# Performance work log

Measured on AMD Instinct MI355X. Metric: run time of the kernel, lower is better.

## Reference

```python
import jax, jax.numpy as jnp
import numpy as np

ALPHA = 0.02
NEG = -9e15

def lrelu(x):
    return jnp.where(x >= 0, x, ALPHA * x)

def layer_norm(x, eps=1e-5):
    m = jnp.mean(x, axis=-1, keepdims=True)
    v = jnp.var(x, axis=-1, keepdims=True)
    return (x - m) * jax.lax.rsqrt(v + eps)

def setup_inputs() -> dict:
    key = jax.random.key(0)
    ks = jax.random.split(key, 10)
    B, N, F_IN, D = 8, 2048, 10, 128
    h = jax.random.normal(ks[0], (B, N, F_IN), jnp.float32)
    adj = jax.random.randint(ks[1], (B, N, N), 0, 2, jnp.int32)
    s = 0.1
    return {
        "h": h,
        "adj": adj,
        "W1": jax.random.normal(ks[2], (D, F_IN), jnp.float32) * s,
        "b1": jax.random.normal(ks[3], (D,), jnp.float32) * s,
        "Wg": jax.random.normal(ks[4], (D, D), jnp.float32) * s,
        "bg": jax.random.normal(ks[5], (D,), jnp.float32) * s,
        "a1": jax.random.normal(ks[6], (D,), jnp.float32) * s,
        "a2": jax.random.normal(ks[7], (D,), jnp.float32) * s,
        "W2": jax.random.normal(ks[8], (2, D), jnp.float32) * s,
        "b2": jax.random.normal(ks[9], (2,), jnp.float32) * s,
    }

def reference(h, adj, W1, b1, Wg, bg, a1, a2, W2, b2):
    # fc1 + layernorm + leakyrelu
    x = h @ W1.T + b1                      # [B,N,128]
    x = lrelu(layer_norm(x))
    # GAT layer
    Wh = x @ Wg.T + bg                     # [B,N,128]
    e1 = Wh @ a1                           # [B,N]
    e2 = Wh @ a2                           # [B,N]
    e = lrelu(e1[:, :, None] + e2[:, None, :])  # [B,N,N]
    e = jnp.where(adj != 0, e, NEG)
    attn = jax.nn.softmax(e, axis=2)
    hp = jnp.einsum('bij,bjd->bid', attn, Wh)    # [B,N,128]
    hp = lrelu(layer_norm(hp))
    # global max pool over nodes
    pooled = jnp.max(hp, axis=1)           # [B,128]
    out = pooled @ W2.T + b2               # [B,2]
    return jax.nn.log_softmax(out, axis=-1)
```

## Files before the change

### kernel.cpp

```cpp
#include <hip/hip_runtime.h>

#define B 8
#define N 2048
#define FIN 10
#define D 128
#define ALPHA 0.02f
#define BR 32
#define TI 32
#define JC 128
#define NBLK_ATTN ((N / TI) * B)

typedef short bf8 __attribute__((ext_vector_type(8)));
typedef short s4v __attribute__((ext_vector_type(4)));
typedef float f32x4 __attribute__((ext_vector_type(4)));

__device__ __forceinline__ float lrelu(float x) { return x >= 0.f ? x : ALPHA * x; }

__device__ __forceinline__ short f2b(float f) {
    unsigned u = __float_as_uint(f);
    return (short)((u + 0x7fffu + ((u >> 16) & 1u)) >> 16);
}

__device__ __forceinline__ float b2f(short s) {
    return __uint_as_float(((unsigned)(unsigned short)s) << 16);
}

__device__ __forceinline__ unsigned enc_key(float v) {
    unsigned b = __float_as_uint(v);
    return (b & 0x80000000u) ? ~b : (b | 0x80000000u);
}
__device__ __forceinline__ float dec_key(unsigned k) {
    unsigned b = (k & 0x80000000u) ? (k & 0x7fffffffu) : ~k;
    return __uint_as_float(b);
}

__global__ __launch_bounds__(256) void k_proj(
    const float* __restrict__ h, const float* __restrict__ W1, const float* __restrict__ b1,
    const float* __restrict__ Wg, const float* __restrict__ bg,
    const float* __restrict__ a1, const float* __restrict__ a2,
    unsigned short* __restrict__ WhT, float* __restrict__ e1g, float* __restrict__ e2g,
    unsigned* __restrict__ pooled, unsigned* __restrict__ cnt)
{
    __shared__ __align__(16) short xep_lds[32 * 136];
    __shared__ __align__(16) short wg_lds[D * 136];
    __shared__ float W1_lds[D * 11];
    __shared__ float h_lds[BR * FIN];
    __shared__ float ep1[2][BR], ep2[2][BR];

    const int t = threadIdx.x;
    const int r0 = blockIdx.x * BR;
    const int bb = r0 >> 11;
    const int jloc = r0 & (N - 1);

    if (blockIdx.x < B && t < D) pooled[blockIdx.x * D + t] = 0u;
    if (blockIdx.x == 0 && t == 128) *cnt = 0u;

    for (int idx = t; idx < D * FIN; idx += 256)
        W1_lds[(idx / FIN) * 11 + (idx % FIN)] = W1[idx];
    for (int idx = t; idx < BR * FIN; idx += 256)
        h_lds[idx] = h[(size_t)r0 * FIN + idx];
    __syncthreads();

    {
        const int dr = t >> 4;
        const int j8 = t & 15;
        #pragma unroll
        for (int pass = 0; pass < 8; pass++) {
            int dd = pass * 16 + dr;
            float4 f0 = *(const float4*)&Wg[dd * D + j8 * 8];
            float4 f1 = *(const float4*)&Wg[dd * D + j8 * 8 + 4];
            bf8 v;
            v[0] = f2b(f0.x); v[1] = f2b(f0.y); v[2] = f2b(f0.z); v[3] = f2b(f0.w);
            v[4] = f2b(f1.x); v[5] = f2b(f1.y); v[6] = f2b(f1.z); v[7] = f2b(f1.w);
            *(bf8*)&wg_lds[dd * 136 + j8 * 8] = v;
        }
    }

    const int w = t >> 6, lane = t & 63;
    {
        float b1v0 = b1[lane], b1v1 = b1[lane + 64];
        for (int i = 0; i < 8; i++) {
            int r = w * 8 + i;
            float s0 = b1v0, s1 = b1v1;
            const float* hr = &h_lds[r * FIN];
            #pragma unroll
            for (int k = 0; k < FIN; k++) {
                float hv = hr[k];
                s0 += hv * W1_lds[lane * 11 + k];
                s1 += hv * W1_lds[(lane + 64) * 11 + k];
            }
            float sm = s0 + s1, sq = s0 * s0 + s1 * s1;
            #pragma unroll
            for (int m = 1; m <= 32; m <<= 1) { sm += __shfl_xor(sm, m); sq += __shfl_xor(sq, m); }
            float mean = sm * (1.f / D);
            float var  = sq * (1.f / D) - mean * mean;
            float rs = rsqrtf(var + 1e-5f);
            xep_lds[r * 136 + lane]      = f2b(lrelu((s0 - mean) * rs));
            xep_lds[r * 136 + lane + 64] = f2b(lrelu((s1 - mean) * rs));
        }
    }
    __syncthreads();

    const int l15 = lane & 15, q = lane >> 4;
    const int mw = w & 1, np = w >> 1;
    f32x4 acc[4];
    #pragma unroll
    for (int nt = 0; nt < 4; nt++)
        #pragma unroll
        for (int r = 0; r < 4; r++) acc[nt][r] = 0.f;

    #pragma unroll
    for (int ks = 0; ks < 4; ks++) {
        bf8 av = *(const bf8*)&xep_lds[(mw * 16 + l15) * 136 + ks * 32 + q * 8];
        #pragma unroll
        for (int nt = 0; nt < 4; nt++) {
            bf8 bv = *(const bf8*)&wg_lds[((np * 4 + nt) * 16 + l15) * 136 + ks * 32 + q * 8];
            acc[nt] = __builtin_amdgcn_mfma_f32_16x16x32_bf16(av, bv, acc[nt], 0, 0, 0);
        }
    }

    float e1p[4] = {0.f, 0.f, 0.f, 0.f}, e2p[4] = {0.f, 0.f, 0.f, 0.f};
    #pragma unroll
    for (int nt = 0; nt < 4; nt++) {
        int col = (np * 4 + nt) * 16 + l15;
        float bgv = bg[col], a1v = a1[col], a2v = a2[col];
        #pragma unroll
        for (int r = 0; r < 4; r++) {
            float v = acc[nt][r] + bgv;
            acc[nt][r] = v;
            e1p[r] += v * a1v;
            e2p[r] += v * a2v;
        }
    }
    #pragma unroll
    for (int m = 1; m <= 8; m <<= 1) {
        #pragma unroll
        for (int r = 0; r < 4; r++) { e1p[r] += __shfl_xor(e1p[r], m); e2p[r] += __shfl_xor(e2p[r], m); }
    }
    if (l15 == 0) {
        #pragma unroll
        for (int r = 0; r < 4; r++) {
            ep1[np][mw * 16 + q * 4 + r] = e1p[r];
            ep2[np][mw * 16 + q * 4 + r] = e2p[r];
        }
    }
    __syncthreads();
    if (t < BR) {
        e1g[r0 + t] = ep1[0][t] + ep1[1][t];
        e2g[r0 + t] = ep2[0][t] + ep2[1][t];
    }
    #pragma unroll
    for (int nt = 0; nt < 4; nt++) {
        int col = (np * 4 + nt) * 16 + l15;
        #pragma unroll
        for (int r = 0; r < 4; r++)
            xep_lds[col * 36 + mw * 16 + q * 4 + r] = f2b(acc[nt][r]);
    }
    __syncthreads();
    {
        const int col = t >> 1, jh = (t & 1) * 16;
        unsigned short* dst = WhT + ((size_t)(bb * D + col)) * N + jloc + jh;
        #pragma unroll
        for (int i2 = 0; i2 < 4; i2++)
            *(uint2*)(dst + i2 * 4) = *(const uint2*)&xep_lds[col * 36 + jh + i2 * 4];
    }
}

__global__ __launch_bounds__(512) void k_attn(
    const int* __restrict__ adj, const unsigned short* __restrict__ WhT,
    const float* __restrict__ e1g, const float* __restrict__ e2g,
    unsigned* __restrict__ pooled, unsigned* __restrict__ cnt,
    const float* __restrict__ W2, const float* __restrict__ b2,
    float* __restrict__ out)
{
    __shared__ __align__(16) short pT[2][TI * 136];
    __shared__ float statsp[4][TI][2];
    __shared__ float maxb[2][D];
    __shared__ float l_lds[TI];
    __shared__ int finalflag;

    const int t = threadIdx.x;
    const int b = blockIdx.y;
    const int i0 = blockIdx.x * TI;

    const int w = t >> 6, lane = t & 63;
    const int l15 = lane & 15, q = lane >> 4;
    const int mw = w & 1;
    const int np = w >> 1;

    const int rg = t >> 5;
    const int jq = (t & 31) * 4;

    const float e1r0 = e1g[b * N + i0 + rg * 2];
    const float e1r1 = e1g[b * N + i0 + rg * 2 + 1];

    const unsigned short* WhTb = WhT + (size_t)b * D * N;
    const int* adjb = adj + ((size_t)b * N + i0) * N;
    const unsigned short* wrow0 = WhTb + (size_t)((np * 2 + 0) * 16 + l15) * N + q * 8;
    const unsigned short* wrow1 = WhTb + (size_t)((np * 2 + 1) * 16 + l15) * N + q * 8;

    f32x4 acc[2];
    #pragma unroll
    for (int nt = 0; nt < 2; nt++)
        #pragma unroll
        for (int r = 0; r < 4; r++) acc[nt][r] = 0.f;
    float ls0 = 0.f, ls1 = 0.f;

    int4 a0 = *(const int4*)(adjb + (size_t)(rg * 2) * N + jq);
    int4 a1r = *(const int4*)(adjb + (size_t)(rg * 2 + 1) * N + jq);
    float4 e2r = *(const float4*)&e2g[b * N + jq];

    for (int jc = 0; jc < N / JC; jc++) {
        bf8 bv0[4], bv1[4];
        #pragma unroll
        for (int ks = 0; ks < 4; ks++) {
            bv0[ks] = *(const bf8*)(wrow0 + jc * JC + ks * 32);
            bv1[ks] = *(const bf8*)(wrow1 + jc * JC + ks * 32);
        }

        short* pTc = &pT[jc & 1][0];

        {
            s4v pv;
            pv[0] = f2b(a0.x ? __expf(lrelu(e1r0 + e2r.x)) : 0.f);
            pv[1] = f2b(a0.y ? __expf(lrelu(e1r0 + e2r.y)) : 0.f);
            pv[2] = f2b(a0.z ? __expf(lrelu(e1r0 + e2r.z)) : 0.f);
            pv[3] = f2b(a0.w ? __expf(lrelu(e1r0 + e2r.w)) : 0.f);
            ls0 += b2f(pv[0]) + b2f(pv[1]) + b2f(pv[2]) + b2f(pv[3]);
            *(s4v*)&pTc[(rg * 2) * 136 + jq] = pv;
            pv[0] = f2b(a1r.x ? __expf(lrelu(e1r1 + e2r.x)) : 0.f);
            pv[1] = f2b(a1r.y ? __expf(lrelu(e1r1 + e2r.y)) : 0.f);
            pv[2] = f2b(a1r.z ? __expf(lrelu(e1r1 + e2r.z)) : 0.f);
            pv[3] = f2b(a1r.w ? __expf(lrelu(e1r1 + e2r.w)) : 0.f);
            ls1 += b2f(pv[0]) + b2f(pv[1]) + b2f(pv[2]) + b2f(pv[3]);
            *(s4v*)&pTc[(rg * 2 + 1) * 136 + jq] = pv;
        }

        if (jc < N / JC - 1) {
            const int j0n = (jc + 1) * JC;
            a0  = *(const int4*)(adjb + (size_t)(rg * 2) * N + j0n + jq);
            a1r = *(const int4*)(adjb + (size_t)(rg * 2 + 1) * N + j0n + jq);
            e2r = *(const float4*)&e2g[b * N + j0n + jq];
        }

        __syncthreads();

        #pragma unroll
        for (int ks = 0; ks < 4; ks++) {
            bf8 av = *(const bf8*)&pTc[(mw * 16 + l15) * 136 + ks * 32 + q * 8];
            acc[0] = __builtin_amdgcn_mfma_f32_16x16x32_bf16(av, bv0[ks], acc[0], 0, 0, 0);
            acc[1] = __builtin_amdgcn_mfma_f32_16x16x32_bf16(av, bv1[ks], acc[1], 0, 0, 0);
        }
    }

    #pragma unroll
    for (int m = 1; m <= 16; m <<= 1) { ls0 += __shfl_xor(ls0, m); ls1 += __shfl_xor(ls1, m); }
    if ((t & 31) == 0) { l_lds[rg * 2] = ls0; l_lds[rg * 2 + 1] = ls1; }
    __syncthreads();

    float smr[4] = {0.f, 0.f, 0.f, 0.f}, sqr[4] = {0.f, 0.f, 0.f, 0.f};
    #pragma unroll
    for (int r = 0; r < 4; r++) {
        float rinv = 1.f / l_lds[mw * 16 + q * 4 + r];
        #pragma unroll
        for (int nt = 0; nt < 2; nt++) {
            float v = acc[nt][r] * rinv;
            acc[nt][r] = v;
            smr[r] += v;
            sqr[r] += v * v;
        }
    }
    #pragma unroll
    for (int m = 1; m <= 8; m <<= 1) {
        #pragma unroll
        for (int r = 0; r < 4; r++) { smr[r] += __shfl_xor(smr[r], m); sqr[r] += __shfl_xor(sqr[r], m); }
    }
    if (l15 == 0) {
        #pragma unroll
        for (int r = 0; r < 4; r++) {
            statsp[np][mw * 16 + q * 4 + r][0] = smr[r];
            statsp[np][mw * 16 + q * 4 + r][1] = sqr[r];
        }
    }
    __syncthreads();

    float mx[2] = {-1e30f, -1e30f};
    #pragma unroll
    for (int r = 0; r < 4; r++) {
        int row = mw * 16 + q * 4 + r;
        float s0 = statsp[0][row][0] + statsp[1][row][0] + statsp[2][row][0] + statsp[3][row][0];
        float s1 = statsp[0][row][1] + statsp[1][row][1] + statsp[2][row][1] + statsp[3][row][1];
        float mean = s0 * (1.f / D);
        float var  = s1 * (1.f / D) - mean * mean;
        float rs = rsqrtf(var + 1e-5f);
        #pragma unroll
        for (int nt = 0; nt < 2; nt++) {
            float v = lrelu((acc[nt][r] - mean) * rs);
            mx[nt] = fmaxf(mx[nt], v);
        }
    }
    #pragma unroll
    for (int m = 16; m <= 32; m <<= 1) {
        #pragma unroll
        for (int nt = 0; nt < 2; nt++) mx[nt] = fmaxf(mx[nt], __shfl_xor(mx[nt], m));
    }
    if (q == 0) {
        #pragma unroll
        for (int nt = 0; nt < 2; nt++) maxb[mw][(np * 2 + nt) * 16 + l15] = mx[nt];
    }
    __syncthreads();
    if (t < D) {
        float v = fmaxf(maxb[0][t], maxb[1][t]);
        atomicMax(&pooled[b * D + t], enc_key(v));
    }
    __syncthreads();

    if (t == 0) {
        __threadfence();
        unsigned old = atomicAdd(cnt, 1u);
        finalflag = (old == NBLK_ATTN - 1) ? 1 : 0;
    }
    __syncthreads();
    if (finalflag && t < 256) {
        const int fb = t >> 5;
        const int fq = t & 31;
        float s0 = 0.f, s1 = 0.f;
        #pragma unroll
        for (int m = 0; m < 4; m++) {
            int dd = fq + 32 * m;
            unsigned key = __hip_atomic_load(&pooled[fb * D + dd], __ATOMIC_RELAXED,
                                             __HIP_MEMORY_SCOPE_AGENT);
            float v = dec_key(key);
            s0 += v * W2[dd];
            s1 += v * W2[D + dd];
        }
        #pragma unroll
        for (int m = 1; m <= 16; m <<= 1) { s0 += __shfl_xor(s0, m); s1 += __shfl_xor(s1, m); }
        if (fq == 0) {
            float o0 = s0 + b2[0], o1 = s1 + b2[1];
            float mxv = fmaxf(o0, o1);
            float ls = logf(__expf(o0 - mxv) + __expf(o1 - mxv));
            out[fb * 2 + 0] = o0 - mxv - ls;
            out[fb * 2 + 1] = o1 - mxv - ls;
        }
    }
}

extern "C" void kernel_launch(void* const* d_in, const int* in_sizes, int n_in,
                              void* d_out, int out_size, void* d_ws, size_t ws_size,
                              hipStream_t stream) {
    const float* h   = (const float*)d_in[0];
    const int*   adj = (const int*)d_in[1];
    const float* W1  = (const float*)d_in[2];
    const float* b1  = (const float*)d_in[3];
    const float* Wg  = (const float*)d_in[4];
    const float* bg  = (const float*)d_in[5];
    const float* a1  = (const float*)d_in[6];
    const float* a2  = (const float*)d_in[7];
    const float* W2  = (const float*)d_in[8];
    const float* b2  = (const float*)d_in[9];
    float* out = (float*)d_out;

    unsigned short* WhT = (unsigned short*)d_ws;
    float* e1g = (float*)((char*)d_ws + (size_t)B * D * N * 2);
    float* e2g = e1g + (size_t)B * N;
    unsigned* pooled = (unsigned*)(e2g + (size_t)B * N);
    unsigned* cnt = pooled + (size_t)B * D;

    k_proj<<<(B * N) / BR, 256, 0, stream>>>(h, W1, b1, Wg, bg, a1, a2,
                                             WhT, e1g, e2g, pooled, cnt);
    k_attn<<<dim3(N / TI, B), 512, 0, stream>>>(adj, WhT, e1g, e2g, pooled, cnt,
                                                W2, b2, out);
}
```

Before: 255.3 us.

## Split attention key dimension across waves and compute P directly in MFMA registers

The attention kernel now uses 16-row tiles with 256 threads. Each of the four waves handles a quarter of the key range and builds its bf16 probability fragment in registers, removing the LDS staging of P and the per-chunk __syncthreads. Partial outputs and row sums are reduced through LDS at the end, and the max-pool is first combined with shared-memory atomics. In exchange, WhT is reread by twice as many blocks, accumulator register pressure is higher (8 MFMA tiles), and the epilogue does more LDS atomics.

```diff
diff --git a/kernel.cpp b/kernel.cpp
--- a/kernel.cpp
+++ b/kernel.cpp
@@ -6,12 +6,11 @@
 #define D 128
 #define ALPHA 0.02f
 #define BR 32
-#define TI 32
-#define JC 128
-#define NBLK_ATTN ((N / TI) * B)
+#define TIA 16
+#define NSTEP (N / 4 / 32)
+#define NBLK_ATTN ((N / TIA) * B)
 
 typedef short bf8 __attribute__((ext_vector_type(8)));
-typedef short s4v __attribute__((ext_vector_type(4)));
 typedef float f32x4 __attribute__((ext_vector_type(4)));
 
 __device__ __forceinline__ float lrelu(float x) { return x >= 0.f ? x : ALPHA * x; }
@@ -166,153 +165,129 @@
     }
 }
 
-__global__ __launch_bounds__(512) void k_attn(
+__global__ __launch_bounds__(256, 4) void k_attn(
     const int* __restrict__ adj, const unsigned short* __restrict__ WhT,
     const float* __restrict__ e1g, const float* __restrict__ e2g,
     unsigned* __restrict__ pooled, unsigned* __restrict__ cnt,
     const float* __restrict__ W2, const float* __restrict__ b2,
     float* __restrict__ out)
 {
-    __shared__ __align__(16) short pT[2][TI * 136];
-    __shared__ float statsp[4][TI][2];
-    __shared__ float maxb[2][D];
-    __shared__ float l_lds[TI];
+    __shared__ float obufp[4][TIA][132];
+    __shared__ float lp[4][TIA];
+    __shared__ unsigned maxd[D];
     __shared__ int finalflag;
 
     const int t = threadIdx.x;
     const int b = blockIdx.y;
-    const int i0 = blockIdx.x * TI;
-
+    const int i0 = blockIdx.x * TIA;
     const int w = t >> 6, lane = t & 63;
     const int l15 = lane & 15, q = lane >> 4;
-    const int mw = w & 1;
-    const int np = w >> 1;
-
-    const int rg = t >> 5;
-    const int jq = (t & 31) * 4;
-
-    const float e1r0 = e1g[b * N + i0 + rg * 2];
-    const float e1r1 = e1g[b * N + i0 + rg * 2 + 1];
-
-    const unsigned short* WhTb = WhT + (size_t)b * D * N;
-    const int* adjb = adj + ((size_t)b * N + i0) * N;
-    const unsigned short* wrow0 = WhTb + (size_t)((np * 2 + 0) * 16 + l15) * N + q * 8;
-    const unsigned short* wrow1 = WhTb + (size_t)((np * 2 + 1) * 16 + l15) * N + q * 8;
-
-    f32x4 acc[2];
-    #pragma unroll
-    for (int nt = 0; nt < 2; nt++)
+
+    if (t < D) maxd[t] = 0u;
+
+    const float e1v = e1g[b * N + i0 + l15];
+    const float* e2b = e2g + (size_t)b * N;
+    const int* adjr = adj + ((size_t)b * N + i0 + l15) * N;
+    const unsigned short* wb = WhT + (size_t)b * D * N + (size_t)l15 * N + q * 8;
+
+    f32x4 acc[8];
+    #pragma unroll
+    for (int nt = 0; nt < 8; nt++)
         #pragma unroll
         for (int r = 0; r < 4; r++) acc[nt][r] = 0.f;
-    float ls0 = 0.f, ls1 = 0.f;
-
-    int4 a0 = *(const int4*)(adjb + (size_t)(rg * 2) * N + jq);
-    int4 a1r = *(const int4*)(adjb + (size_t)(rg * 2 + 1) * N + jq);
-    float4 e2r = *(const float4*)&e2g[b * N + jq];
-
-    for (int jc = 0; jc < N / JC; jc++) {
-        bf8 bv0[4], bv1[4];
-        #pragma unroll
-        for (int ks = 0; ks < 4; ks++) {
-            bv0[ks] = *(const bf8*)(wrow0 + jc * JC + ks * 32);
-            bv1[ks] = *(const bf8*)(wrow1 + jc * JC + ks * 32);
-        }
-
-        short* pTc = &pT[jc & 1][0];
-
-        {
-            s4v pv;
-            pv[0] = f2b(a0.x ? __expf(lrelu(e1r0 + e2r.x)) : 0.f);
-            pv[1] = f2b(a0.y ? __expf(lrelu(e1r0 + e2r.y)) : 0.f);
-            pv[2] = f2b(a0.z ? __expf(lrelu(e1r0 + e2r.z)) : 0.f);
-            pv[3] = f2b(a0.w ? __expf(lrelu(e1r0 + e2r.w)) : 0.f);
-            ls0 += b2f(pv[0]) + b2f(pv[1]) + b2f(pv[2]) + b2f(pv[3]);
-            *(s4v*)&pTc[(rg * 2) * 136 + jq] = pv;
-            pv[0] = f2b(a1r.x ? __expf(lrelu(e1r1 + e2r.x)) : 0.f);
-            pv[1] = f2b(a1r.y ? __expf(lrelu(e1r1 + e2r.y)) : 0.f);
-            pv[2] = f2b(a1r.z ? __expf(lrelu(e1r1 + e2r.z)) : 0.f);
-            pv[3] = f2b(a1r.w ? __expf(lrelu(e1r1 + e2r.w)) : 0.f);
-            ls1 += b2f(pv[0]) + b2f(pv[1]) + b2f(pv[2]) + b2f(pv[3]);
-            *(s4v*)&pTc[(rg * 2 + 1) * 136 + jq] = pv;
-        }
-
-        if (jc < N / JC - 1) {
-            const int j0n = (jc + 1) * JC;
-            a0  = *(const int4*)(adjb + (size_t)(rg * 2) * N + j0n + jq);
-            a1r = *(const int4*)(adjb + (size_t)(rg * 2 + 1) * N + j0n + jq);
-            e2r = *(const float4*)&e2g[b * N + j0n + jq];
-        }
-
-        __syncthreads();
-
-        #pragma unroll
-        for (int ks = 0; ks < 4; ks++) {
-            bf8 av = *(const bf8*)&pTc[(mw * 16 + l15) * 136 + ks * 32 + q * 8];
-            acc[0] = __builtin_amdgcn_mfma_f32_16x16x32_bf16(av, bv0[ks], acc[0], 0, 0, 0);
-            acc[1] = __builtin_amdgcn_mfma_f32_16x16x32_bf16(av, bv1[ks], acc[1], 0, 0, 0);
-        }
-    }
-
-    #pragma unroll
-    for (int m = 1; m <= 16; m <<= 1) { ls0 += __shfl_xor(ls0, m); ls1 += __shfl_xor(ls1, m); }
-    if ((t & 31) == 0) { l_lds[rg * 2] = ls0; l_lds[rg * 2 + 1] = ls1; }
-    __syncthreads();
-
-    float smr[4] = {0.f, 0.f, 0.f, 0.f}, sqr[4] = {0.f, 0.f, 0.f, 0.f};
-    #pragma unroll
-    for (int r = 0; r < 4; r++) {
-        float rinv = 1.f / l_lds[mw * 16 + q * 4 + r];
-        #pragma unroll
-        for (int nt = 0; nt < 2; nt++) {
-            float v = acc[nt][r] * rinv;
-            acc[nt][r] = v;
-            smr[r] += v;
-            sqr[r] += v * v;
-        }
-    }
-    #pragma unroll
-    for (int m = 1; m <= 8; m <<= 1) {
-        #pragma unroll
-        for (int r = 0; r < 4; r++) { smr[r] += __shfl_xor(smr[r], m); sqr[r] += __shfl_xor(sqr[r], m); }
-    }
-    if (l15 == 0) {
-        #pragma unroll
-        for (int r = 0; r < 4; r++) {
-            statsp[np][mw * 16 + q * 4 + r][0] = smr[r];
-            statsp[np][mw * 16 + q * 4 + r][1] = sqr[r];
-        }
-    }
-    __syncthreads();
-
-    float mx[2] = {-1e30f, -1e30f};
-    #pragma unroll
-    for (int r = 0; r < 4; r++) {
-        int row = mw * 16 + q * 4 + r;
-        float s0 = statsp[0][row][0] + statsp[1][row][0] + statsp[2][row][0] + statsp[3][row][0];
-        float s1 = statsp[0][row][1] + statsp[1][row][1] + statsp[2][row][1] + statsp[3][row][1];
-        float mean = s0 * (1.f / D);
-        float var  = s1 * (1.f / D) - mean * mean;
+    float ls = 0.f;
+
+    const int jw0 = w * (N / 4);
+    const int jq8 = q * 8;
+
+    int4 aa = *(const int4*)(adjr + jw0 + jq8);
+    int4 ab = *(const int4*)(adjr + jw0 + jq8 + 4);
+    float4 ea = *(const float4*)(e2b + jw0 + jq8);
+    float4 eb = *(const float4*)(e2b + jw0 + jq8 + 4);
+
+    for (int js = 0; js < NSTEP; js++) {
+        const int jbase = jw0 + js * 32;
+        const unsigned short* wbj = wb + jbase;
+
+        bf8 bv[8];
+        #pragma unroll
+        for (int nt = 0; nt < 8; nt++)
+            bv[nt] = *(const bf8*)(wbj + (size_t)nt * 16 * N);
+
+        int4 na = aa, nb_ = ab;
+        float4 nea = ea, neb = eb;
+        if (js + 1 < NSTEP) {
+            const int jn = jbase + 32;
+            na  = *(const int4*)(adjr + jn + jq8);
+            nb_ = *(const int4*)(adjr + jn + jq8 + 4);
+            nea = *(const float4*)(e2b + jn + jq8);
+            neb = *(const float4*)(e2b + jn + jq8 + 4);
+        }
+
+        bf8 av;
+        av[0] = f2b(aa.x ? __expf(lrelu(e1v + ea.x)) : 0.f);
+        av[1] = f2b(aa.y ? __expf(lrelu(e1v + ea.y)) : 0.f);
+        av[2] = f2b(aa.z ? __expf(lrelu(e1v + ea.z)) : 0.f);
+        av[3] = f2b(aa.w ? __expf(lrelu(e1v + ea.w)) : 0.f);
+        av[4] = f2b(ab.x ? __expf(lrelu(e1v + eb.x)) : 0.f);
+        av[5] = f2b(ab.y ? __expf(lrelu(e1v + eb.y)) : 0.f);
+        av[6] = f2b(ab.z ? __expf(lrelu(e1v + eb.z)) : 0.f);
+        av[7] = f2b(ab.w ? __expf(lrelu(e1v + eb.w)) : 0.f);
+        ls += b2f(av[0]) + b2f(av[1]) + b2f(av[2]) + b2f(av[3])
+            + b2f(av[4]) + b2f(av[5]) + b2f(av[6]) + b2f(av[7]);
+
+        #pragma unroll
+        for (int nt = 0; nt < 8; nt++)
+            acc[nt] = __builtin_amdgcn_mfma_f32_16x16x32_bf16(av, bv[nt], acc[nt], 0, 0, 0);
+
+        aa = na; ab = nb_; ea = nea; eb = neb;
+    }
+
+    ls += __shfl_xor(ls, 16);
+    ls += __shfl_xor(ls, 32);
+    if (lane < 16) lp[w][lane] = ls;
+
+    #pragma unroll
+    for (int nt = 0; nt < 8; nt++)
+        #pragma unroll
+        for (int r = 0; r < 4; r++)
+            obufp[w][q * 4 + r][nt * 16 + l15] = acc[nt][r];
+    __syncthreads();
+
+    {
+        const int ri = t >> 4;
+        const int c  = t & 15;
+        const int dbase = c * 8;
+        float lsum = lp[0][ri] + lp[1][ri] + lp[2][ri] + lp[3][ri];
+        float rinv = 1.f / lsum;
+        float o[8];
+        #pragma unroll
+        for (int k = 0; k < 8; k += 4) {
+            float4 s0 = *(const float4*)&obufp[0][ri][dbase + k];
+            float4 s1 = *(const float4*)&obufp[1][ri][dbase + k];
+            float4 s2 = *(const float4*)&obufp[2][ri][dbase + k];
+            float4 s3 = *(const float4*)&obufp[3][ri][dbase + k];
+            o[k + 0] = (s0.x + s1.x + s2.x + s3.x) * rinv;
+            o[k + 1] = (s0.y + s1.y + s2.y + s3.y) * rinv;
+            o[k + 2] = (s0.z + s1.z + s2.z + s3.z) * rinv;
+            o[k + 3] = (s0.w + s1.w + s2.w + s3.w) * rinv;
+        }
+        float sm = 0.f, sq = 0.f;
+        #pragma unroll
+        for (int k = 0; k < 8; k++) { sm += o[k]; sq += o[k] * o[k]; }
+        #pragma unroll
+        for (int m = 1; m <= 8; m <<= 1) { sm += __shfl_xor(sm, m); sq += __shfl_xor(sq, m); }
+        float mean = sm * (1.f / D);
+        float var  = sq * (1.f / D) - mean * mean;
         float rs = rsqrtf(var + 1e-5f);
         #pragma unroll
-        for (int nt = 0; nt < 2; nt++) {
-            float v = lrelu((acc[nt][r] - mean) * rs);
-            mx[nt] = fmaxf(mx[nt], v);
-        }
-    }
-    #pragma unroll
-    for (int m = 16; m <= 32; m <<= 1) {
-        #pragma unroll
-        for (int nt = 0; nt < 2; nt++) mx[nt] = fmaxf(mx[nt], __shfl_xor(mx[nt], m));
-    }
-    if (q == 0) {
-        #pragma unroll
-        for (int nt = 0; nt < 2; nt++) maxb[mw][(np * 2 + nt) * 16 + l15] = mx[nt];
-    }
-    __syncthreads();
-    if (t < D) {
-        float v = fmaxf(maxb[0][t], maxb[1][t]);
-        atomicMax(&pooled[b * D + t], enc_key(v));
-    }
+        for (int k = 0; k < 8; k++) {
+            float v = lrelu((o[k] - mean) * rs);
+            atomicMax(&maxd[dbase + k], enc_key(v));
+        }
+    }
+    __syncthreads();
+    if (t < D) atomicMax(&pooled[b * D + t], maxd[t]);
     __syncthreads();
 
     if (t == 0) {
@@ -339,9 +314,9 @@
         if (fq == 0) {
             float o0 = s0 + b2[0], o1 = s1 + b2[1];
             float mxv = fmaxf(o0, o1);
-            float ls = logf(__expf(o0 - mxv) + __expf(o1 - mxv));
-            out[fb * 2 + 0] = o0 - mxv - ls;
-            out[fb * 2 + 1] = o1 - mxv - ls;
+            float ls2 = logf(__expf(o0 - mxv) + __expf(o1 - mxv));
+            out[fb * 2 + 0] = o0 - mxv - ls2;
+            out[fb * 2 + 1] = o1 - mxv - ls2;
         }
     }
 }
@@ -369,6 +344,6 @@
 
     k_proj<<<(B * N) / BR, 256, 0, stream>>>(h, W1, b1, Wg, bg, a1, a2,
                                              WhT, e1g, e2g, pooled, cnt);
-    k_attn<<<dim3(N / TI, B), 512, 0, stream>>>(adj, WhT, e1g, e2g, pooled, cnt,
-                                                W2, b2, out);
-}
+    k_attn<<<dim3(N / TIA, B), 256, 0, stream>>>(adj, WhT, e1g, e2g, pooled, cnt,
+                                                 W2, b2, out);
+}
```

Measured after the change: 311.3 us. 1.22x slower.

## Stage WhT, adj and e2 tiles into LDS via direct global-to-LDS DMA

Applied to the files above, without the earlier changes.

The attention kernel now copies the WhT chunk, the adjacency tile and the e2 slice into LDS with global_load_lds, instead of loading them into registers. The WhT tile is stored with an XOR swizzle to avoid LDS bank conflicts, and adj/e2 are double-buffered. Manual vmcnt waits, sched barriers and setprio around the MFMA block control the overlap. The aim is to cut register pressure and global-load latency stalls so more waves fit per CU (launch bounds 512,4), at the cost of much higher LDS use and fragile hand-counted waitcnt synchronisation.

```diff
diff --git a/kernel.cpp b/kernel.cpp
--- a/kernel.cpp
+++ b/kernel.cpp
@@ -8,10 +8,10 @@
 #define BR 32
 #define TI 32
 #define JC 128
+#define NCH (N / JC)
 #define NBLK_ATTN ((N / TI) * B)
 
 typedef short bf8 __attribute__((ext_vector_type(8)));
-typedef short s4v __attribute__((ext_vector_type(4)));
 typedef float f32x4 __attribute__((ext_vector_type(4)));
 
 __device__ __forceinline__ float lrelu(float x) { return x >= 0.f ? x : ALPHA * x; }
@@ -32,6 +32,17 @@
 __device__ __forceinline__ float dec_key(unsigned k) {
     unsigned b = (k & 0x80000000u) ? (k & 0x7fffffffu) : ~k;
     return __uint_as_float(b);
+}
+
+__device__ __forceinline__ void dma16(const void* g, void* l) {
+    __builtin_amdgcn_global_load_lds(
+        (const __attribute__((address_space(1))) void*)g,
+        (__attribute__((address_space(3))) void*)l, 16, 0, 0);
+}
+__device__ __forceinline__ void dma4(const void* g, void* l) {
+    __builtin_amdgcn_global_load_lds(
+        (const __attribute__((address_space(1))) void*)g,
+        (__attribute__((address_space(3))) void*)l, 4, 0, 0);
 }
 
 __global__ __launch_bounds__(256) void k_proj(
@@ -166,14 +177,17 @@
     }
 }
 
-__global__ __launch_bounds__(512) void k_attn(
+__global__ __launch_bounds__(512, 4) void k_attn(
     const int* __restrict__ adj, const unsigned short* __restrict__ WhT,
     const float* __restrict__ e1g, const float* __restrict__ e2g,
     unsigned* __restrict__ pooled, unsigned* __restrict__ cnt,
     const float* __restrict__ W2, const float* __restrict__ b2,
     float* __restrict__ out)
 {
-    __shared__ __align__(16) short pT[2][TI * 136];
+    __shared__ __align__(16) short whTL[D * JC];
+    __shared__ __align__(16) int   adjL[2][TI * JC];
+    __shared__ __align__(16) float e2L[2][JC];
+    __shared__ __align__(16) short pT[TI * 136];
     __shared__ float statsp[4][TI][2];
     __shared__ float maxb[2][D];
     __shared__ float l_lds[TI];
@@ -188,74 +202,111 @@
     const int mw = w & 1;
     const int np = w >> 1;
 
-    const int rg = t >> 5;
-    const int jq = (t & 31) * 4;
-
-    const float e1r0 = e1g[b * N + i0 + rg * 2];
-    const float e1r1 = e1g[b * N + i0 + rg * 2 + 1];
-
+    const int sel = lane >> 4;
+    const int c16 = lane & 15;
+    const int row_a = 2 * w + ((sel >> 1) << 4) + (sel & 1);
+
+    const float e1row = e1g[b * N + i0 + row_a];
     const unsigned short* WhTb = WhT + (size_t)b * D * N;
     const int* adjb = adj + ((size_t)b * N + i0) * N;
-    const unsigned short* wrow0 = WhTb + (size_t)((np * 2 + 0) * 16 + l15) * N + q * 8;
-    const unsigned short* wrow1 = WhTb + (size_t)((np * 2 + 1) * 16 + l15) * N + q * 8;
+    const float* e2b = e2g + (size_t)b * N;
 
     f32x4 acc[2];
     #pragma unroll
     for (int nt = 0; nt < 2; nt++)
         #pragma unroll
         for (int r = 0; r < 4; r++) acc[nt][r] = 0.f;
-    float ls0 = 0.f, ls1 = 0.f;
-
-    int4 a0 = *(const int4*)(adjb + (size_t)(rg * 2) * N + jq);
-    int4 a1r = *(const int4*)(adjb + (size_t)(rg * 2 + 1) * N + jq);
-    float4 e2r = *(const float4*)&e2g[b * N + jq];
-
-    for (int jc = 0; jc < N / JC; jc++) {
-        bf8 bv0[4], bv1[4];
+    float ls = 0.f;
+
+    auto stage_whT = [&](int jc) {
+        #pragma unroll
+        for (int p = 0; p < 4; p++) {
+            int x = p * 8192 + w * 1024 + lane * 16;
+            int rowx = x >> 8;
+            int scol = (x & 255) ^ ((rowx & 7) << 4);
+            dma16((const char*)WhTb + (size_t)rowx * (N * 2) + jc * (JC * 2) + scol,
+                  (char*)whTL + x);
+        }
+    };
+    auto stage_adj = [&](int jcn, int buf) {
+        #pragma unroll
+        for (int p = 0; p < 2; p++) {
+            int y = p * 8192 + w * 1024 + lane * 16;
+            int rowy = y >> 9;
+            dma16((const char*)adjb + (size_t)rowy * (N * 4) + jcn * (JC * 4) + (y & 511),
+                  (char*)&adjL[buf][0] + y);
+        }
+    };
+    auto stage_e2 = [&](int jcn, int buf) {
+        dma4((const char*)e2b + jcn * (JC * 4) + lane * 4,
+             (char*)&e2L[buf][0] + lane * 4);
+        dma4((const char*)e2b + jcn * (JC * 4) + 256 + lane * 4,
+             (char*)&e2L[buf][0] + 256 + lane * 4);
+    };
+
+    stage_adj(0, 0);
+    stage_e2(0, 0);
+
+    for (int jc = 0; jc < NCH; jc++) {
+        const int cb = jc & 1;
+        const int jn = (jc + 1) & (NCH - 1);
+
+        stage_whT(jc);
+        stage_adj(jn, cb ^ 1);
+        stage_e2(jn, cb ^ 1);
+
+        asm volatile("s_waitcnt vmcnt(8)" ::: "memory");
+        __builtin_amdgcn_sched_barrier(0);
+
+        {
+            const char* abase = (char*)&adjL[cb][0]
+                + ((sel >> 1) << 13) + w * 1024 + ((sel & 1) << 9) + c16 * 32;
+            int4 av0 = *(const int4*)abase;
+            int4 av1 = *(const int4*)(abase + 16);
+            const char* ebase = (char*)&e2L[cb][0] + c16 * 32;
+            float4 ev0 = *(const float4*)ebase;
+            float4 ev1 = *(const float4*)(ebase + 16);
+            bf8 pv;
+            pv[0] = f2b(av0.x ? __expf(lrelu(e1row + ev0.x)) : 0.f);
+            pv[1] = f2b(av0.y ? __expf(lrelu(e1row + ev0.y)) : 0.f);
+            pv[2] = f2b(av0.z ? __expf(lrelu(e1row + ev0.z)) : 0.f);
+            pv[3] = f2b(av0.w ? __expf(lrelu(e1row + ev0.w)) : 0.f);
+            pv[4] = f2b(av1.x ? __expf(lrelu(e1row + ev1.x)) : 0.f);
+            pv[5] = f2b(av1.y ? __expf(lrelu(e1row + ev1.y)) : 0.f);
+            pv[6] = f2b(av1.z ? __expf(lrelu(e1row + ev1.z)) : 0.f);
+            pv[7] = f2b(av1.w ? __expf(lrelu(e1row + ev1.w)) : 0.f);
+            ls += b2f(pv[0]) + b2f(pv[1]) + b2f(pv[2]) + b2f(pv[3])
+                + b2f(pv[4]) + b2f(pv[5]) + b2f(pv[6]) + b2f(pv[7]);
+            *(bf8*)&pT[row_a * 136 + c16 * 8] = pv;
+        }
+
+        asm volatile("s_waitcnt vmcnt(4) lgkmcnt(0)" ::: "memory");
+        __builtin_amdgcn_sched_barrier(0);
+        __builtin_amdgcn_s_barrier();
+
+        __builtin_amdgcn_s_setprio(1);
         #pragma unroll
         for (int ks = 0; ks < 4; ks++) {
-            bv0[ks] = *(const bf8*)(wrow0 + jc * JC + ks * 32);
-            bv1[ks] = *(const bf8*)(wrow1 + jc * JC + ks * 32);
-        }
-
-        short* pTc = &pT[jc & 1][0];
-
-        {
-            s4v pv;
-            pv[0] = f2b(a0.x ? __expf(lrelu(e1r0 + e2r.x)) : 0.f);
-            pv[1] = f2b(a0.y ? __expf(lrelu(e1r0 + e2r.y)) : 0.f);
-            pv[2] = f2b(a0.z ? __expf(lrelu(e1r0 + e2r.z)) : 0.f);
-            pv[3] = f2b(a0.w ? __expf(lrelu(e1r0 + e2r.w)) : 0.f);
-            ls0 += b2f(pv[0]) + b2f(pv[1]) + b2f(pv[2]) + b2f(pv[3]);
-            *(s4v*)&pTc[(rg * 2) * 136 + jq] = pv;
-            pv[0] = f2b(a1r.x ? __expf(lrelu(e1r1 + e2r.x)) : 0.f);
-            pv[1] = f2b(a1r.y ? __expf(lrelu(e1r1 + e2r.y)) : 0.f);
-            pv[2] = f2b(a1r.z ? __expf(lrelu(e1r1 + e2r.z)) : 0.f);
-            pv[3] = f2b(a1r.w ? __expf(lrelu(e1r1 + e2r.w)) : 0.f);
-            ls1 += b2f(pv[0]) + b2f(pv[1]) + b2f(pv[2]) + b2f(pv[3]);
-            *(s4v*)&pTc[(rg * 2 + 1) * 136 + jq] = pv;
-        }
-
-        if (jc < N / JC - 1) {
-            const int j0n = (jc + 1) * JC;
-            a0  = *(const int4*)(adjb + (size_t)(rg * 2) * N + j0n + jq);
-            a1r = *(const int4*)(adjb + (size_t)(rg * 2 + 1) * N + j0n + jq);
-            e2r = *(const float4*)&e2g[b * N + j0n + jq];
-        }
-
-        __syncthreads();
-
-        #pragma unroll
-        for (int ks = 0; ks < 4; ks++) {
-            bf8 av = *(const bf8*)&pTc[(mw * 16 + l15) * 136 + ks * 32 + q * 8];
-            acc[0] = __builtin_amdgcn_mfma_f32_16x16x32_bf16(av, bv0[ks], acc[0], 0, 0, 0);
-            acc[1] = __builtin_amdgcn_mfma_f32_16x16x32_bf16(av, bv1[ks], acc[1], 0, 0, 0);
-        }
-    }
-
-    #pragma unroll
-    for (int m = 1; m <= 16; m <<= 1) { ls0 += __shfl_xor(ls0, m); ls1 += __shfl_xor(ls1, m); }
-    if ((t & 31) == 0) { l_lds[rg * 2] = ls0; l_lds[rg * 2 + 1] = ls1; }
+            bf8 av = *(const bf8*)&pT[(mw * 16 + l15) * 136 + ks * 32 + q * 8];
+            #pragma unroll
+            for (int nt = 0; nt < 2; nt++) {
+                int rowb = (np * 2 + nt) * 16 + l15;
+                const bf8* bp = (const bf8*)((char*)whTL + rowb * 256
+                                  + (((ks * 64 + q * 16) ^ ((l15 & 7) << 4))));
+                acc[nt] = __builtin_amdgcn_mfma_f32_16x16x32_bf16(av, *bp, acc[nt], 0, 0, 0);
+            }
+        }
+        __builtin_amdgcn_s_setprio(0);
+
+        asm volatile("s_waitcnt lgkmcnt(0)" ::: "memory");
+        __builtin_amdgcn_sched_barrier(0);
+        __builtin_amdgcn_s_barrier();
+    }
+    asm volatile("s_waitcnt vmcnt(0)" ::: "memory");
+
+    #pragma unroll
+    for (int m = 1; m <= 8; m <<= 1) ls += __shfl_xor(ls, m);
+    if (c16 == 0) l_lds[row_a] = ls;
     __syncthreads();
 
     float smr[4] = {0.f, 0.f, 0.f, 0.f}, sqr[4] = {0.f, 0.f, 0.f, 0.f};
@@ -339,9 +390,9 @@
         if (fq == 0) {
             float o0 = s0 + b2[0], o1 = s1 + b2[1];
             float mxv = fmaxf(o0, o1);
-            float ls = logf(__expf(o0 - mxv) + __expf(o1 - mxv));
-            out[fb * 2 + 0] = o0 - mxv - ls;
-            out[fb * 2 + 1] = o1 - mxv - ls;
+            float ls2 = logf(__expf(o0 - mxv) + __expf(o1 - mxv));
+            out[fb * 2 + 0] = o0 - mxv - ls2;
+            out[fb * 2 + 1] = o1 - mxv - ls2;
         }
     }
 }
```

Result: faster. 235.3 us, median of 2 (-7.8%).
